# Optimization experiments

Measured on AMD Instinct MI355X. Metric: run time of the kernel, lower is better.

## Reference

```python
import jax, jax.numpy as jnp
import numpy as np

B, N, F, F_PRIME, H = 16, 256, 64, 16, 128  # H = hidden width hardcoded as 128 in source


def _pairwise_dist(r):
    # torch.cdist(r, r), p=2. r: [B,N,3] -> [B,N,N]
    diff = r[:, :, None, :] - r[:, None, :, :]          # [B,N,N,3]
    sq = jnp.sum(diff * diff, axis=-1)                  # [B,N,N]
    safe = jnp.where(sq > 0, sq, 1.0)
    return jnp.where(sq > 0, jnp.sqrt(safe), 0.0)


def setup_inputs() -> dict:
    key = jax.random.key(0)
    ks = jax.random.split(key, 10)
    s = lambda fan_in: 1.0 / np.sqrt(fan_in)
    return {
        "r_batch": jax.random.uniform(ks[0], (B, N, 3), jnp.float32),
        "f_batch": jax.random.uniform(ks[1], (B, N, F), jnp.float32),
        # MessagePassingLayer MLP: 1 -> 128 -> F (weights stored [in, out])
        "mp_w1": jax.random.uniform(ks[2], (1, H), jnp.float32, -s(1), s(1)),
        "mp_b1": jax.random.uniform(ks[3], (H,), jnp.float32, -s(1), s(1)),
        "mp_w2": jax.random.uniform(ks[4], (H, F), jnp.float32, -s(H), s(H)),
        "mp_b2": jax.random.uniform(ks[5], (F,), jnp.float32, -s(H), s(H)),
        # PointwiseConvolutionLayer MLP: F -> 128 -> F_prime
        "pc_w1": jax.random.uniform(ks[6], (F, H), jnp.float32, -s(F), s(F)),
        "pc_b1": jax.random.uniform(ks[7], (H,), jnp.float32, -s(F), s(F)),
        "pc_w2": jax.random.uniform(ks[8], (H, F_PRIME), jnp.float32, -s(H), s(H)),
        "pc_b2": jax.random.uniform(ks[9], (F_PRIME,), jnp.float32, -s(H), s(H)),
    }


def reference(r_batch, f_batch, mp_w1, mp_b1, mp_w2, mp_b2, pc_w1, pc_b1, pc_w2, pc_b2):
    sp = jax.nn.softplus
    d = _pairwise_dist(r_batch)                                   # [B,N,N]
    # per-pair MLP on scalar distance: 1 -> 128 -> F
    hidden = sp(d[..., None] * mp_w1[0] + mp_b1)                  # [B,N,N,H]
    d_prime = sp(jnp.einsum('bijh,hf->bijf', hidden, mp_w2) + mp_b2)  # [B,N,N,F]
    # matmul + diagonal == per-feature weighted sum over neighbors j
    f_bar = sp(jnp.einsum('bijf,bjf->bif', d_prime, f_batch))     # [B,N,F]
    # pointwise MLP: F -> 128 -> F_prime
    h2 = sp(jnp.einsum('bnf,fh->bnh', f_bar, pc_w1) + pc_b1)      # [B,N,H]
    return sp(jnp.einsum('bnh,hp->bnp', h2, pc_w2) + pc_b2)       # [B,N,F_prime]
```

## Files before the change

### kernel.cpp

```cpp
#include <hip/hip_runtime.h>
#include <math.h>

#define B_   16
#define N_   256
#define F_   64
#define FP_  16
#define H_   128
#define K_   14
#define M_   128
#define DMAX 1.7320508075688772f
#define PI_F 3.14159265358979323846f
#define LROW 264

typedef _Float16 h16;
typedef __attribute__((ext_vector_type(2))) _Float16 h16x2;
typedef __attribute__((ext_vector_type(8))) _Float16 h16x8;
typedef __attribute__((ext_vector_type(4))) float    f32x4;

__device__ __forceinline__ float sp(float x) {
    return fmaxf(x, 0.0f) + log1pf(expf(-fabsf(x)));
}

__global__ void pp_vals(const float* __restrict__ mp_w1, const float* __restrict__ mp_b1,
                        const float* __restrict__ mp_w2, const float* __restrict__ mp_b2,
                        float* __restrict__ vals) {
    __shared__ float hid[H_];
    const int m = blockIdx.x, tid = threadIdx.x;
    const float th = PI_F * ((float)m + 0.5f) / (float)M_;
    const float d  = (cosf(th) + 1.0f) * 0.5f * DMAX;
    hid[tid] = sp(fmaf(d, mp_w1[tid], mp_b1[tid]));
    __syncthreads();
    if (tid < F_) {
        float z = mp_b2[tid];
        #pragma unroll 8
        for (int h = 0; h < H_; ++h)
            z = fmaf(hid[h], mp_w2[h * F_ + tid], z);
        vals[m * F_ + tid] = sp(z);
    }
}

__global__ void pp_fit(const float* __restrict__ vals, float* __restrict__ c) {
    __shared__ float part[4][F_];
    const int k   = blockIdx.x;
    const int tid = threadIdx.x;
    const int f   = tid & 63;
    const int g   = tid >> 6;
    float s = 0.0f;
    #pragma unroll 8
    for (int mm = 0; mm < M_ / 4; ++mm) {
        const int m = g * (M_ / 4) + mm;
        const float th = PI_F * ((float)m + 0.5f) / (float)M_;
        s = fmaf(vals[m * F_ + f], __cosf((float)k * th), s);
    }
    part[g][f] = s;
    __syncthreads();
    if (tid < F_) {
        const float t = part[0][f] + part[1][f] + part[2][f] + part[3][f];
        c[k * F_ + f] = (k == 0) ? t / (float)M_ : 2.0f * t / (float)M_;
    }
}

__global__ __launch_bounds__(256) void pp_fbar_mfma(
        const float* __restrict__ r, const float* __restrict__ fb,
        const float* __restrict__ c, float* __restrict__ fbar_out) {
    const int tid = threadIdx.x;
    const int b   = blockIdx.x >> 4;
    const int i0  = (blockIdx.x & 15) << 4;

    __shared__ h16   s_x[16 * LROW];
    __shared__ h16   s_fbT[F_ * LROW];
    __shared__ float s_c[K_ * F_];
    __shared__ float s_part[4][16 * 68];
    __shared__ float s_ri[16 * 3];

    if (tid < 48) s_ri[tid] = r[((size_t)b * N_ + i0) * 3 + tid];
    for (int p = 0; p < 4; ++p) {
        const int idx = p * 256 + tid;
        if (idx < K_ * F_) s_c[idx] = c[idx];
    }
    {
        const float* fbb = fb + (size_t)b * N_ * F_;
        const int f4 = tid & 15;
        const int jp = tid >> 4;
        #pragma unroll
        for (int jb = 0; jb < 8; ++jb) {
            const int j0 = jb * 32 + jp * 2;
            const float4 v0 = *(const float4*)(fbb + (size_t)j0 * F_ + f4 * 4);
            const float4 v1 = *(const float4*)(fbb + (size_t)(j0 + 1) * F_ + f4 * 4);
            const float a0[4] = {v0.x, v0.y, v0.z, v0.w};
            const float a1[4] = {v1.x, v1.y, v1.z, v1.w};
            #pragma unroll
            for (int ff = 0; ff < 4; ++ff) {
                h16x2 pk; pk.x = (h16)a0[ff]; pk.y = (h16)a1[ff];
                *(h16x2*)&s_fbT[(f4 * 4 + ff) * LROW + j0] = pk;
            }
        }
    }
    __syncthreads();

    {
        const int j = tid;
        const float xj = r[((size_t)b * N_ + j) * 3 + 0];
        const float yj = r[((size_t)b * N_ + j) * 3 + 1];
        const float zj = r[((size_t)b * N_ + j) * 3 + 2];
        const float sc = 2.0f / DMAX;
        #pragma unroll
        for (int m = 0; m < 16; ++m) {
            const float dx = s_ri[m * 3 + 0] - xj;
            const float dy = s_ri[m * 3 + 1] - yj;
            const float dz = s_ri[m * 3 + 2] - zj;
            const float sq = fmaf(dx, dx, fmaf(dy, dy, dz * dz));
            const float d  = sq > 0.0f ? sqrtf(sq) : 0.0f;
            s_x[m * LROW + j] = (h16)(fmaf(d, sc, -1.0f));
        }
    }
    __syncthreads();

    const int wv   = tid >> 6;
    const int lane = tid & 63;
    const int ln   = lane & 15;
    const int q    = lane >> 4;

    h16x8 bfrag[2][4];
    h16x8 x8[2];
    #pragma unroll
    for (int cc = 0; cc < 2; ++cc) {
        const int j0 = wv * 64 + cc * 32;
        x8[cc] = *(const h16x8*)&s_x[ln * LROW + j0 + q * 8];
        #pragma unroll
        for (int ft = 0; ft < 4; ++ft)
            bfrag[cc][ft] = *(const h16x8*)&s_fbT[(ft * 16 + ln) * LROW + j0 + q * 8];
    }

    h16x8 ones, twox[2], ta[2], tb[2];
    #pragma unroll
    for (int e = 0; e < 8; ++e) ones[e] = (h16)1.0f;
    #pragma unroll
    for (int cc = 0; cc < 2; ++cc) {
        twox[cc] = x8[cc] + x8[cc];
        ta[cc] = ones;
        tb[cc] = x8[cc];
    }

    f32x4 facc[4];
    #pragma unroll
    for (int ft = 0; ft < 4; ++ft) facc[ft] = (f32x4){0.f, 0.f, 0.f, 0.f};
    const f32x4 z4 = (f32x4){0.f, 0.f, 0.f, 0.f};

    for (int k = 0; k < K_; ++k) {
        f32x4 acc[4];
        #pragma unroll
        for (int ft = 0; ft < 4; ++ft) {
            acc[ft] = __builtin_amdgcn_mfma_f32_16x16x32_f16(ta[0], bfrag[0][ft], z4, 0, 0, 0);
            acc[ft] = __builtin_amdgcn_mfma_f32_16x16x32_f16(ta[1], bfrag[1][ft], acc[ft], 0, 0, 0);
        }
        #pragma unroll
        for (int ft = 0; ft < 4; ++ft) {
            const float ck = s_c[k * F_ + ft * 16 + ln];
            facc[ft].x = fmaf(ck, acc[ft].x, facc[ft].x);
            facc[ft].y = fmaf(ck, acc[ft].y, facc[ft].y);
            facc[ft].z = fmaf(ck, acc[ft].z, facc[ft].z);
            facc[ft].w = fmaf(ck, acc[ft].w, facc[ft].w);
        }
        #pragma unroll
        for (int cc = 0; cc < 2; ++cc) {
            const h16x8 tn = twox[cc] * tb[cc] - ta[cc];
            ta[cc] = tb[cc];
            tb[cc] = tn;
        }
    }

    #pragma unroll
    for (int ft = 0; ft < 4; ++ft) {
        const float v[4] = {facc[ft].x, facc[ft].y, facc[ft].z, facc[ft].w};
        #pragma unroll
        for (int rr = 0; rr < 4; ++rr)
            s_part[wv][(q * 4 + rr) * 68 + ft * 16 + ln] = v[rr];
    }
    __syncthreads();

    {
        const int f  = tid & 63;
        const int ig = tid >> 6;
        #pragma unroll
        for (int p = 0; p < 4; ++p) {
            const int i = ig * 4 + p;
            const float s = s_part[0][i * 68 + f] + s_part[1][i * 68 + f]
                          + s_part[2][i * 68 + f] + s_part[3][i * 68 + f];
            fbar_out[((size_t)(b * N_ + i0 + i)) * F_ + f] = sp(s);
        }
    }
}

__global__ __launch_bounds__(256) void pp_mlp(
        const float* __restrict__ fbar,
        const float* __restrict__ pc_w1, const float* __restrict__ pc_b1,
        const float* __restrict__ pc_w2, const float* __restrict__ pc_b2,
        float* __restrict__ out) {
    const int tid  = threadIdx.x;
    const int row0 = blockIdx.x * 2;

    __shared__ float s_fb[2 * F_];
    __shared__ float s_h2[2 * H_];

    if (tid < 2 * F_)
        s_fb[tid] = fbar[(size_t)row0 * F_ + tid];
    __syncthreads();

    {
        const int ii = tid >> 7, h = tid & 127;
        float z = pc_b1[h];
        #pragma unroll 8
        for (int f = 0; f < F_; ++f)
            z = fmaf(s_fb[ii * F_ + f], pc_w1[f * H_ + h], z);
        s_h2[tid] = sp(z);
    }
    __syncthreads();

    if (tid < 2 * FP_) {
        const int ii = tid >> 4, p = tid & 15;
        float z = pc_b2[p];
        #pragma unroll 8
        for (int h = 0; h < H_; ++h)
            z = fmaf(s_h2[ii * H_ + h], pc_w2[h * FP_ + p], z);
        out[(size_t)(row0 + ii) * FP_ + p] = sp(z);
    }
}

extern "C" void kernel_launch(void* const* d_in, const int* in_sizes, int n_in,
                              void* d_out, int out_size, void* d_ws, size_t ws_size,
                              hipStream_t stream) {
    const float* r_batch = (const float*)d_in[0];
    const float* f_batch = (const float*)d_in[1];
    const float* mp_w1   = (const float*)d_in[2];
    const float* mp_b1   = (const float*)d_in[3];
    const float* mp_w2   = (const float*)d_in[4];
    const float* mp_b2   = (const float*)d_in[5];
    const float* pc_w1   = (const float*)d_in[6];
    const float* pc_b1   = (const float*)d_in[7];
    const float* pc_w2   = (const float*)d_in[8];
    const float* pc_b2   = (const float*)d_in[9];
    float* out = (float*)d_out;

    float* vals = (float*)d_ws;
    float* chb  = (float*)((char*)d_ws + 32768);
    float* fbar = (float*)((char*)d_ws + 65536);

    pp_vals<<<M_, H_, 0, stream>>>(mp_w1, mp_b1, mp_w2, mp_b2, vals);
    pp_fit<<<K_, 256, 0, stream>>>(vals, chb);
    pp_fbar_mfma<<<B_ * (N_ / 16), 256, 0, stream>>>(r_batch, f_batch, chb, fbar);
    pp_mlp<<<B_ * N_ / 2, 256, 0, stream>>>(fbar, pc_w1, pc_b1, pc_w2, pc_b2, out);
}
```

Measured before the change: 100.3 us.

## Split neighbor dimension across two blocks and reduce partials in MLP kernel

Result: no change. 99.60 us (-0.7%).

```diff
diff --git a/kernel.cpp b/kernel.cpp
--- a/kernel.cpp
+++ b/kernel.cpp
@@ -10,7 +10,8 @@
 #define M_   128
 #define DMAX 1.7320508075688772f
 #define PI_F 3.14159265358979323846f
-#define LROW 264
+#define JL   128
+#define LRJ  136
 
 typedef _Float16 h16;
 typedef __attribute__((ext_vector_type(2))) _Float16 h16x2;
@@ -62,28 +63,32 @@
 
 __global__ __launch_bounds__(256) void pp_fbar_mfma(
         const float* __restrict__ r, const float* __restrict__ fb,
-        const float* __restrict__ c, float* __restrict__ fbar_out) {
+        const float* __restrict__ c, float* __restrict__ part_out) {
     const int tid = threadIdx.x;
-    const int b   = blockIdx.x >> 4;
-    const int i0  = (blockIdx.x & 15) << 4;
-
-    __shared__ h16   s_x[16 * LROW];
-    __shared__ h16   s_fbT[F_ * LROW];
+    const int b   = blockIdx.x >> 5;
+    const int w   = blockIdx.x & 31;
+    const int i0  = (w >> 1) << 4;
+    const int jh  = w & 1;
+
+    __shared__ h16   s_x[16 * LRJ];
+    __shared__ __align__(16) char s_mem[F_ * LRJ * 2];
     __shared__ float s_c[K_ * F_];
-    __shared__ float s_part[4][16 * 68];
     __shared__ float s_ri[16 * 3];
+    h16*   s_fbT  = (h16*)s_mem;
+    float* s_part = (float*)s_mem;
 
     if (tid < 48) s_ri[tid] = r[((size_t)b * N_ + i0) * 3 + tid];
+    #pragma unroll
     for (int p = 0; p < 4; ++p) {
         const int idx = p * 256 + tid;
         if (idx < K_ * F_) s_c[idx] = c[idx];
     }
     {
-        const float* fbb = fb + (size_t)b * N_ * F_;
+        const float* fbb = fb + ((size_t)b * N_ + jh * JL) * F_;
         const int f4 = tid & 15;
         const int jp = tid >> 4;
         #pragma unroll
-        for (int jb = 0; jb < 8; ++jb) {
+        for (int jb = 0; jb < 4; ++jb) {
             const int j0 = jb * 32 + jp * 2;
             const float4 v0 = *(const float4*)(fbb + (size_t)j0 * F_ + f4 * 4);
             const float4 v1 = *(const float4*)(fbb + (size_t)(j0 + 1) * F_ + f4 * 4);
@@ -92,26 +97,29 @@
             #pragma unroll
             for (int ff = 0; ff < 4; ++ff) {
                 h16x2 pk; pk.x = (h16)a0[ff]; pk.y = (h16)a1[ff];
-                *(h16x2*)&s_fbT[(f4 * 4 + ff) * LROW + j0] = pk;
+                *(h16x2*)&s_fbT[(f4 * 4 + ff) * LRJ + j0] = pk;
             }
         }
     }
     __syncthreads();
 
     {
-        const int j = tid;
-        const float xj = r[((size_t)b * N_ + j) * 3 + 0];
-        const float yj = r[((size_t)b * N_ + j) * 3 + 1];
-        const float zj = r[((size_t)b * N_ + j) * 3 + 2];
+        const int lj   = tid & 127;
+        const int half = tid >> 7;
+        const int gj   = jh * JL + lj;
+        const float xj = r[((size_t)b * N_ + gj) * 3 + 0];
+        const float yj = r[((size_t)b * N_ + gj) * 3 + 1];
+        const float zj = r[((size_t)b * N_ + gj) * 3 + 2];
         const float sc = 2.0f / DMAX;
         #pragma unroll
-        for (int m = 0; m < 16; ++m) {
+        for (int mm = 0; mm < 8; ++mm) {
+            const int m = half * 8 + mm;
             const float dx = s_ri[m * 3 + 0] - xj;
             const float dy = s_ri[m * 3 + 1] - yj;
             const float dz = s_ri[m * 3 + 2] - zj;
             const float sq = fmaf(dx, dx, fmaf(dy, dy, dz * dz));
             const float d  = sq > 0.0f ? sqrtf(sq) : 0.0f;
-            s_x[m * LROW + j] = (h16)(fmaf(d, sc, -1.0f));
+            s_x[m * LRJ + lj] = (h16)(fmaf(d, sc, -1.0f));
         }
     }
     __syncthreads();
@@ -120,27 +128,21 @@
     const int lane = tid & 63;
     const int ln   = lane & 15;
     const int q    = lane >> 4;
-
-    h16x8 bfrag[2][4];
-    h16x8 x8[2];
-    #pragma unroll
-    for (int cc = 0; cc < 2; ++cc) {
-        const int j0 = wv * 64 + cc * 32;
-        x8[cc] = *(const h16x8*)&s_x[ln * LROW + j0 + q * 8];
-        #pragma unroll
-        for (int ft = 0; ft < 4; ++ft)
-            bfrag[cc][ft] = *(const h16x8*)&s_fbT[(ft * 16 + ln) * LROW + j0 + q * 8];
-    }
-
-    h16x8 ones, twox[2], ta[2], tb[2];
+    const int jo   = wv * 32 + q * 8;
+
+    const h16x8 x8 = *(const h16x8*)&s_x[ln * LRJ + jo];
+    h16x8 bfrag[4];
+    #pragma unroll
+    for (int ft = 0; ft < 4; ++ft)
+        bfrag[ft] = *(const h16x8*)&s_fbT[(ft * 16 + ln) * LRJ + jo];
+    __syncthreads();
+
+    h16x8 ones, twox, ta, tb;
     #pragma unroll
     for (int e = 0; e < 8; ++e) ones[e] = (h16)1.0f;
-    #pragma unroll
-    for (int cc = 0; cc < 2; ++cc) {
-        twox[cc] = x8[cc] + x8[cc];
-        ta[cc] = ones;
-        tb[cc] = x8[cc];
-    }
+    twox = x8 + x8;
+    ta = ones;
+    tb = x8;
 
     f32x4 facc[4];
     #pragma unroll
@@ -148,26 +150,18 @@
     const f32x4 z4 = (f32x4){0.f, 0.f, 0.f, 0.f};
 
     for (int k = 0; k < K_; ++k) {
-        f32x4 acc[4];
         #pragma unroll
         for (int ft = 0; ft < 4; ++ft) {
-            acc[ft] = __builtin_amdgcn_mfma_f32_16x16x32_f16(ta[0], bfrag[0][ft], z4, 0, 0, 0);
-            acc[ft] = __builtin_amdgcn_mfma_f32_16x16x32_f16(ta[1], bfrag[1][ft], acc[ft], 0, 0, 0);
-        }
-        #pragma unroll
-        for (int ft = 0; ft < 4; ++ft) {
+            const f32x4 acc = __builtin_amdgcn_mfma_f32_16x16x32_f16(ta, bfrag[ft], z4, 0, 0, 0);
             const float ck = s_c[k * F_ + ft * 16 + ln];
-            facc[ft].x = fmaf(ck, acc[ft].x, facc[ft].x);
-            facc[ft].y = fmaf(ck, acc[ft].y, facc[ft].y);
-            facc[ft].z = fmaf(ck, acc[ft].z, facc[ft].z);
-            facc[ft].w = fmaf(ck, acc[ft].w, facc[ft].w);
-        }
-        #pragma unroll
-        for (int cc = 0; cc < 2; ++cc) {
-            const h16x8 tn = twox[cc] * tb[cc] - ta[cc];
-            ta[cc] = tb[cc];
-            tb[cc] = tn;
-        }
+            facc[ft].x = fmaf(ck, acc.x, facc[ft].x);
+            facc[ft].y = fmaf(ck, acc.y, facc[ft].y);
+            facc[ft].z = fmaf(ck, acc.z, facc[ft].z);
+            facc[ft].w = fmaf(ck, acc.w, facc[ft].w);
+        }
+        const h16x8 tn = twox * tb - ta;
+        ta = tb;
+        tb = tn;
     }
 
     #pragma unroll
@@ -175,7 +169,7 @@
         const float v[4] = {facc[ft].x, facc[ft].y, facc[ft].z, facc[ft].w};
         #pragma unroll
         for (int rr = 0; rr < 4; ++rr)
-            s_part[wv][(q * 4 + rr) * 68 + ft * 16 + ln] = v[rr];
+            s_part[(wv * 16 + q * 4 + rr) * 68 + ft * 16 + ln] = v[rr];
     }
     __syncthreads();
 
@@ -185,15 +179,15 @@
         #pragma unroll
         for (int p = 0; p < 4; ++p) {
             const int i = ig * 4 + p;
-            const float s = s_part[0][i * 68 + f] + s_part[1][i * 68 + f]
-                          + s_part[2][i * 68 + f] + s_part[3][i * 68 + f];
-            fbar_out[((size_t)(b * N_ + i0 + i)) * F_ + f] = sp(s);
+            const float s = s_part[(0 * 16 + i) * 68 + f] + s_part[(1 * 16 + i) * 68 + f]
+                          + s_part[(2 * 16 + i) * 68 + f] + s_part[(3 * 16 + i) * 68 + f];
+            part_out[(size_t)jh * (B_ * N_ * F_) + ((size_t)(b * N_ + i0 + i)) * F_ + f] = s;
         }
     }
 }
 
 __global__ __launch_bounds__(256) void pp_mlp(
-        const float* __restrict__ fbar,
+        const float* __restrict__ part,
         const float* __restrict__ pc_w1, const float* __restrict__ pc_b1,
         const float* __restrict__ pc_w2, const float* __restrict__ pc_b2,
         float* __restrict__ out) {
@@ -203,8 +197,10 @@
     __shared__ float s_fb[2 * F_];
     __shared__ float s_h2[2 * H_];
 
-    if (tid < 2 * F_)
-        s_fb[tid] = fbar[(size_t)row0 * F_ + tid];
+    if (tid < 2 * F_) {
+        const size_t idx = (size_t)row0 * F_ + tid;
+        s_fb[tid] = sp(part[idx] + part[(size_t)B_ * N_ * F_ + idx]);
+    }
     __syncthreads();
 
     {
@@ -244,10 +240,10 @@
 
     float* vals = (float*)d_ws;
     float* chb  = (float*)((char*)d_ws + 32768);
-    float* fbar = (float*)((char*)d_ws + 65536);
+    float* part = (float*)((char*)d_ws + 65536);
 
     pp_vals<<<M_, H_, 0, stream>>>(mp_w1, mp_b1, mp_w2, mp_b2, vals);
     pp_fit<<<K_, 256, 0, stream>>>(vals, chb);
-    pp_fbar_mfma<<<B_ * (N_ / 16), 256, 0, stream>>>(r_batch, f_batch, chb, fbar);
-    pp_mlp<<<B_ * N_ / 2, 256, 0, stream>>>(fbar, pc_w1, pc_b1, pc_w2, pc_b2, out);
-}
+    pp_fbar_mfma<<<B_ * (N_ / 16) * 2, 256, 0, stream>>>(r_batch, f_batch, chb, part);
+    pp_mlp<<<B_ * N_ / 2, 256, 0, stream>>>(part, pc_w1, pc_b1, pc_w2, pc_b2, out);
+}
```
